# Optimization experiments

Measured on AMD Instinct MI355X. Metric: run time of the kernel, lower is better.

The kernel has to match this reference:

```python
import jax, jax.numpy as jnp
import numpy as np

N = 4096
D = 2048
NUM_CLASSES = 128
MARGIN = 0.5


def setup_inputs() -> dict:
    key = jax.random.key(0)
    k1, k2, k3 = jax.random.split(key, 3)
    modal1_inputs = jax.random.normal(k1, (N, D), dtype=jnp.float32)
    modal2_inputs = jax.random.normal(k2, (N, D), dtype=jnp.float32)
    targets = jax.random.randint(k3, (N,), 0, NUM_CLASSES, dtype=jnp.int32)
    return {"modal1_inputs": modal1_inputs, "modal2_inputs": modal2_inputs, "targets": targets}


def _segment_mean(x, seg_ids, num_segments):
    sums = jax.ops.segment_sum(x, seg_ids, num_segments=num_segments)
    cnts = jax.ops.segment_sum(jnp.ones((x.shape[0],), x.dtype), seg_ids, num_segments=num_segments)
    return sums / jnp.maximum(cnts, 1.0)[:, None]


def _pairwise_dist(a, b):
    # sqrt of clamped squared Euclidean distance, matching compute_dist
    sq = (jnp.sum(a * a, axis=1)[:, None] + jnp.sum(b * b, axis=1)[None, :]
          - 2.0 * jnp.einsum('nd,md->nm', a, b))
    return jnp.sqrt(jnp.maximum(sq, 1e-12))


def _contrastive(d2, d1, label, margin):
    # mean(label * d2^2 + (1-label) * relu(margin - d1)^2)
    return jnp.mean(label * d2 * d2
                    + (1.0 - label) * jnp.square(jnp.maximum(margin - d1, 0.0)))


def reference(modal1_inputs, modal2_inputs, targets):
    # per-label means (segment mean), gathered back per-sample as in the loop
    meanR = _segment_mean(modal1_inputs, targets, NUM_CLASSES)  # [C, D]
    meanT = _segment_mean(modal2_inputs, targets, NUM_CLASSES)  # [C, D]
    centersR = meanR[targets]                                   # [N, D]
    centersT = meanT[targets]                                   # [N, D]
    centers = 0.5 * (centersR + centersT)                       # [N, D]

    label = (targets[:, None] == targets[None, :]).astype(jnp.float32)  # [N, N]

    dist1 = _pairwise_dist(centersR, centers)  # already sqrt'ed, per original
    dist2 = _pairwise_dist(centersT, centers)
    dd1 = jnp.sqrt(dist1 + 1e-10)              # sqrt of sqrt, per original
    dd2 = jnp.sqrt(dist2 + 1e-10)

    loss1 = _contrastive(dist1, dd1, label, MARGIN)
    loss2 = _contrastive(dist2, dd2, label, MARGIN)
    return loss1 + loss2
```

## Files before the change

kernel.cpp:

```cpp
#include <hip/hip_runtime.h>

#define N_SAMPLES 4096
#define DIM 2048
#define NUM_CLASSES 128
#define MARGIN 0.5f


__global__ __launch_bounds__(256) void mean_kernel(
        const float* __restrict__ x1,
        const float* __restrict__ x2,
        const int* __restrict__ targets,
        int* __restrict__ cnt,
        float* __restrict__ meanR,
        float* __restrict__ meanT,
        float* __restrict__ d_out, int out_size) {
    __shared__ int s_rows[N_SAMPLES];
    __shared__ int s_n;
    const int tid = threadIdx.x;
    const int c = blockIdx.y;
    const float* __restrict__ x = (blockIdx.z == 0) ? x1 : x2;
    float* __restrict__ mean    = (blockIdx.z == 0) ? meanR : meanT;

    if (tid == 0) s_n = 0;
    if (blockIdx.x == 0 && blockIdx.y == 0 && blockIdx.z == 0) {
        for (int i = tid; i < out_size; i += 256) d_out[i] = 0.0f;
    }
    __syncthreads();

    const int4* __restrict__ t4 = (const int4*)targets;
    for (int i = tid; i < N_SAMPLES / 4; i += 256) {
        const int4 v = t4[i];
        const int base = i * 4;
        if (v.x == c) s_rows[atomicAdd(&s_n, 1)] = base;
        if (v.y == c) s_rows[atomicAdd(&s_n, 1)] = base + 1;
        if (v.z == c) s_rows[atomicAdd(&s_n, 1)] = base + 2;
        if (v.w == c) s_rows[atomicAdd(&s_n, 1)] = base + 3;
    }
    __syncthreads();
    const int n = s_n;

    const int col = blockIdx.x * 256 + tid;
    const float4* __restrict__ xs = (const float4*)x;
    float ax = 0.0f, ay = 0.0f, az = 0.0f, aw = 0.0f;
    int k = 0;
    for (; k + 4 <= n; k += 4) {
        const int r0 = s_rows[k + 0];
        const int r1 = s_rows[k + 1];
        const int r2 = s_rows[k + 2];
        const int r3 = s_rows[k + 3];
        const float4 v0 = xs[(size_t)r0 * (DIM / 4) + col];
        const float4 v1 = xs[(size_t)r1 * (DIM / 4) + col];
        const float4 v2 = xs[(size_t)r2 * (DIM / 4) + col];
        const float4 v3 = xs[(size_t)r3 * (DIM / 4) + col];
        ax += (v0.x + v1.x) + (v2.x + v3.x);
        ay += (v0.y + v1.y) + (v2.y + v3.y);
        az += (v0.z + v1.z) + (v2.z + v3.z);
        aw += (v0.w + v1.w) + (v2.w + v3.w);
    }
    for (; k < n; ++k) {
        const int r = s_rows[k];
        const float4 v = xs[(size_t)r * (DIM / 4) + col];
        ax += v.x; ay += v.y; az += v.z; aw += v.w;
    }
    const float inv = 1.0f / (float)((n > 0) ? n : 1);
    float4 m; m.x = ax * inv; m.y = ay * inv; m.z = az * inv; m.w = aw * inv;
    ((float4*)mean)[(size_t)c * (DIM / 4) + col] = m;

    if (blockIdx.x == 0 && blockIdx.z == 0 && tid == 0) cnt[c] = n;
}

__device__ __forceinline__ void accum_sq(float& acc, const float4& a, const float4& c) {
    float d;
    d = a.x - c.x; acc = fmaf(d, d, acc);
    d = a.y - c.y; acc = fmaf(d, d, acc);
    d = a.z - c.z; acc = fmaf(d, d, acc);
    d = a.w - c.w; acc = fmaf(d, d, acc);
}

__device__ __forceinline__ float wave_sum64(float v) {
#pragma unroll
    for (int m = 32; m >= 1; m >>= 1) v += __shfl_xor(v, m, 64);
    return v;
}

__global__ __launch_bounds__(256) void loss_kernel(
        const float* __restrict__ meanR,
        const float* __restrict__ meanT,
        const int* __restrict__ cnt,
        float* __restrict__ d_out) {
    const int gtid = blockIdx.x * blockDim.x + threadIdx.x;
    const int wid  = gtid >> 6;
    const int lane = threadIdx.x & 63;
    const int a0 = (wid >> 5) * 4;
    const int b0 = (wid & 31) * 4;

    float acc1[4][4], acc2[4][4];
#pragma unroll
    for (int i = 0; i < 4; ++i)
#pragma unroll
        for (int j = 0; j < 4; ++j) { acc1[i][j] = 0.0f; acc2[i][j] = 0.0f; }

    const int ITERS = DIM / 4 / 64;
#pragma unroll 2
    for (int it = 0; it < ITERS; ++it) {
        const int d = lane + it * 64;
        float4 ra[4], ta[4];
#pragma unroll
        for (int i = 0; i < 4; ++i) {
            ra[i] = ((const float4*)(meanR + (size_t)(a0 + i) * DIM))[d];
            ta[i] = ((const float4*)(meanT + (size_t)(a0 + i) * DIM))[d];
        }
#pragma unroll
        for (int j = 0; j < 4; ++j) {
            const int b = b0 + j;
            const float4 rb = ((const float4*)(meanR + (size_t)b * DIM))[d];
            const float4 tb = ((const float4*)(meanT + (size_t)b * DIM))[d];
            float4 cb;
            cb.x = 0.5f * (rb.x + tb.x);
            cb.y = 0.5f * (rb.y + tb.y);
            cb.z = 0.5f * (rb.z + tb.z);
            cb.w = 0.5f * (rb.w + tb.w);
#pragma unroll
            for (int i = 0; i < 4; ++i) {
                accum_sq(acc1[i][j], ra[i], cb);
                accum_sq(acc2[i][j], ta[i], cb);
            }
        }
    }

#pragma unroll
    for (int i = 0; i < 4; ++i)
#pragma unroll
        for (int j = 0; j < 4; ++j) {
            acc1[i][j] = wave_sum64(acc1[i][j]);
            acc2[i][j] = wave_sum64(acc2[i][j]);
        }

    __shared__ float s_part[4];
    if (lane == 0) {
        const float invN2 = 1.0f / ((float)N_SAMPLES * (float)N_SAMPLES);
        float total = 0.0f;
#pragma unroll
        for (int i = 0; i < 4; ++i) {
            const int a = a0 + i;
            const float ca = (float)cnt[a];
#pragma unroll
            for (int j = 0; j < 4; ++j) {
                const int b = b0 + j;
                const float w = ca * (float)cnt[b] * invN2;
                const float sq1 = fmaxf(acc1[i][j], 1e-12f);
                const float sq2 = fmaxf(acc2[i][j], 1e-12f);
                float t1, t2;
                if (a == b) {
                    t1 = sq1;
                    t2 = sq2;
                } else {
                    const float dd1 = sqrtf(sqrtf(sq1) + 1e-10f);
                    const float dd2 = sqrtf(sqrtf(sq2) + 1e-10f);
                    const float r1 = fmaxf(MARGIN - dd1, 0.0f);
                    const float r2 = fmaxf(MARGIN - dd2, 0.0f);
                    t1 = r1 * r1;
                    t2 = r2 * r2;
                }
                total += w * (t1 + t2);
            }
        }
        s_part[threadIdx.x >> 6] = total;
    }
    __syncthreads();
    if (threadIdx.x == 0)
        atomicAdd(d_out, (s_part[0] + s_part[1]) + (s_part[2] + s_part[3]));
}

extern "C" void kernel_launch(void* const* d_in, const int* in_sizes, int n_in,
                              void* d_out, int out_size, void* d_ws, size_t ws_size,
                              hipStream_t stream) {
    const float* modal1 = (const float*)d_in[0];
    const float* modal2 = (const float*)d_in[1];
    const int* targets  = (const int*)d_in[2];
    float* out = (float*)d_out;

    char* ws = (char*)d_ws;
    int*   cnt   = (int*)(ws + 0);
    float* meanR = (float*)(ws + 1024);
    float* meanT = (float*)(ws + 1024 + (size_t)NUM_CLASSES * DIM * 4);

    dim3 gridB(2, NUM_CLASSES, 2);
    mean_kernel<<<gridB, 256, 0, stream>>>(modal1, modal2, targets, cnt,
                                           meanR, meanT, out, out_size);

    const int waves = (NUM_CLASSES / 4) * (NUM_CLASSES / 4);
    loss_kernel<<<waves / 4, 256, 0, stream>>>(meanR, meanT, cnt, out);
}
```

Baseline: 119.7 us.

## Software-pipeline mean gather loads and split loss tiles across block waves

The mean kernel's gather loop now processes eight rows per step and issues the next group's loads before summing the current group, so more memory requests are in flight per thread. The loss kernel gives each 4x4 class tile its own block, splits the feature dimension across four waves, and combines the partial sums through shared memory. This launches four times as many blocks, each doing a quarter of the reduction work, which improves occupancy and latency hiding. The cost is more registers in the mean kernel plus an extra shared-memory reduction and barrier per block.

New measurement: 115.4 us. 3.6% less time.

```diff
diff --git a/kernel.cpp b/kernel.cpp
--- a/kernel.cpp
+++ b/kernel.cpp
@@ -42,26 +42,56 @@
     const int col = blockIdx.x * 256 + tid;
     const float4* __restrict__ xs = (const float4*)x;
     float ax = 0.0f, ay = 0.0f, az = 0.0f, aw = 0.0f;
+
     int k = 0;
-    for (; k + 4 <= n; k += 4) {
-        const int r0 = s_rows[k + 0];
-        const int r1 = s_rows[k + 1];
-        const int r2 = s_rows[k + 2];
-        const int r3 = s_rows[k + 3];
-        const float4 v0 = xs[(size_t)r0 * (DIM / 4) + col];
-        const float4 v1 = xs[(size_t)r1 * (DIM / 4) + col];
-        const float4 v2 = xs[(size_t)r2 * (DIM / 4) + col];
-        const float4 v3 = xs[(size_t)r3 * (DIM / 4) + col];
-        ax += (v0.x + v1.x) + (v2.x + v3.x);
-        ay += (v0.y + v1.y) + (v2.y + v3.y);
-        az += (v0.z + v1.z) + (v2.z + v3.z);
-        aw += (v0.w + v1.w) + (v2.w + v3.w);
+    const int body = n & ~7;
+    if (body >= 8) {
+        int r0 = s_rows[0], r1 = s_rows[1], r2 = s_rows[2], r3 = s_rows[3];
+        int r4 = s_rows[4], r5 = s_rows[5], r6 = s_rows[6], r7 = s_rows[7];
+        float4 v0 = xs[(size_t)r0 * (DIM / 4) + col];
+        float4 v1 = xs[(size_t)r1 * (DIM / 4) + col];
+        float4 v2 = xs[(size_t)r2 * (DIM / 4) + col];
+        float4 v3 = xs[(size_t)r3 * (DIM / 4) + col];
+        float4 v4 = xs[(size_t)r4 * (DIM / 4) + col];
+        float4 v5 = xs[(size_t)r5 * (DIM / 4) + col];
+        float4 v6 = xs[(size_t)r6 * (DIM / 4) + col];
+        float4 v7 = xs[(size_t)r7 * (DIM / 4) + col];
+
+#pragma unroll 1
+        for (k = 8; k + 8 <= body; k += 8) {
+            const int q0 = s_rows[k + 0], q1 = s_rows[k + 1];
+            const int q2 = s_rows[k + 2], q3 = s_rows[k + 3];
+            const int q4 = s_rows[k + 4], q5 = s_rows[k + 5];
+            const int q6 = s_rows[k + 6], q7 = s_rows[k + 7];
+            const float4 w0 = xs[(size_t)q0 * (DIM / 4) + col];
+            const float4 w1 = xs[(size_t)q1 * (DIM / 4) + col];
+            const float4 w2 = xs[(size_t)q2 * (DIM / 4) + col];
+            const float4 w3 = xs[(size_t)q3 * (DIM / 4) + col];
+            const float4 w4 = xs[(size_t)q4 * (DIM / 4) + col];
+            const float4 w5 = xs[(size_t)q5 * (DIM / 4) + col];
+            const float4 w6 = xs[(size_t)q6 * (DIM / 4) + col];
+            const float4 w7 = xs[(size_t)q7 * (DIM / 4) + col];
+
+            ax += ((v0.x + v1.x) + (v2.x + v3.x)) + ((v4.x + v5.x) + (v6.x + v7.x));
+            ay += ((v0.y + v1.y) + (v2.y + v3.y)) + ((v4.y + v5.y) + (v6.y + v7.y));
+            az += ((v0.z + v1.z) + (v2.z + v3.z)) + ((v4.z + v5.z) + (v6.z + v7.z));
+            aw += ((v0.w + v1.w) + (v2.w + v3.w)) + ((v4.w + v5.w) + (v6.w + v7.w));
+
+            v0 = w0; v1 = w1; v2 = w2; v3 = w3;
+            v4 = w4; v5 = w5; v6 = w6; v7 = w7;
+        }
+        ax += ((v0.x + v1.x) + (v2.x + v3.x)) + ((v4.x + v5.x) + (v6.x + v7.x));
+        ay += ((v0.y + v1.y) + (v2.y + v3.y)) + ((v4.y + v5.y) + (v6.y + v7.y));
+        az += ((v0.z + v1.z) + (v2.z + v3.z)) + ((v4.z + v5.z) + (v6.z + v7.z));
+        aw += ((v0.w + v1.w) + (v2.w + v3.w)) + ((v4.w + v5.w) + (v6.w + v7.w));
+        k = body;
     }
     for (; k < n; ++k) {
         const int r = s_rows[k];
         const float4 v = xs[(size_t)r * (DIM / 4) + col];
         ax += v.x; ay += v.y; az += v.z; aw += v.w;
     }
+
     const float inv = 1.0f / (float)((n > 0) ? n : 1);
     float4 m; m.x = ax * inv; m.y = ay * inv; m.z = az * inv; m.w = aw * inv;
     ((float4*)mean)[(size_t)c * (DIM / 4) + col] = m;
@@ -88,11 +118,11 @@
         const float* __restrict__ meanT,
         const int* __restrict__ cnt,
         float* __restrict__ d_out) {
-    const int gtid = blockIdx.x * blockDim.x + threadIdx.x;
-    const int wid  = gtid >> 6;
+    const int tile = blockIdx.x;
+    const int a0 = (tile >> 5) * 4;
+    const int b0 = (tile & 31) * 4;
+    const int wave = threadIdx.x >> 6;
     const int lane = threadIdx.x & 63;
-    const int a0 = (wid >> 5) * 4;
-    const int b0 = (wid & 31) * 4;
 
     float acc1[4][4], acc2[4][4];
 #pragma unroll
@@ -100,10 +130,9 @@
 #pragma unroll
         for (int j = 0; j < 4; ++j) { acc1[i][j] = 0.0f; acc2[i][j] = 0.0f; }
 
-    const int ITERS = DIM / 4 / 64;
-#pragma unroll 2
-    for (int it = 0; it < ITERS; ++it) {
-        const int d = lane + it * 64;
+#pragma unroll
+    for (int it = 0; it < 2; ++it) {
+        const int d = wave * 128 + it * 64 + lane;
         float4 ra[4], ta[4];
 #pragma unroll
         for (int i = 0; i < 4; ++i) {
@@ -136,40 +165,47 @@
             acc2[i][j] = wave_sum64(acc2[i][j]);
         }
 
-    __shared__ float s_part[4];
+    __shared__ float s1[4][16], s2[4][16];
     if (lane == 0) {
-        const float invN2 = 1.0f / ((float)N_SAMPLES * (float)N_SAMPLES);
+#pragma unroll
+        for (int i = 0; i < 4; ++i)
+#pragma unroll
+            for (int j = 0; j < 4; ++j) {
+                s1[wave][i * 4 + j] = acc1[i][j];
+                s2[wave][i * 4 + j] = acc2[i][j];
+            }
+    }
+    __syncthreads();
+
+    if (threadIdx.x < 64) {
         float total = 0.0f;
-#pragma unroll
-        for (int i = 0; i < 4; ++i) {
-            const int a = a0 + i;
-            const float ca = (float)cnt[a];
-#pragma unroll
-            for (int j = 0; j < 4; ++j) {
-                const int b = b0 + j;
-                const float w = ca * (float)cnt[b] * invN2;
-                const float sq1 = fmaxf(acc1[i][j], 1e-12f);
-                const float sq2 = fmaxf(acc2[i][j], 1e-12f);
-                float t1, t2;
-                if (a == b) {
-                    t1 = sq1;
-                    t2 = sq2;
-                } else {
-                    const float dd1 = sqrtf(sqrtf(sq1) + 1e-10f);
-                    const float dd2 = sqrtf(sqrtf(sq2) + 1e-10f);
-                    const float r1 = fmaxf(MARGIN - dd1, 0.0f);
-                    const float r2 = fmaxf(MARGIN - dd2, 0.0f);
-                    t1 = r1 * r1;
-                    t2 = r2 * r2;
-                }
-                total += w * (t1 + t2);
+        if (threadIdx.x < 16) {
+            const int idx = threadIdx.x;
+            const int i = idx >> 2, j = idx & 3;
+            const int a = a0 + i, b = b0 + j;
+            const float sqa1 = (s1[0][idx] + s1[1][idx]) + (s1[2][idx] + s1[3][idx]);
+            const float sqa2 = (s2[0][idx] + s2[1][idx]) + (s2[2][idx] + s2[3][idx]);
+            const float invN2 = 1.0f / ((float)N_SAMPLES * (float)N_SAMPLES);
+            const float w = (float)cnt[a] * (float)cnt[b] * invN2;
+            const float sq1 = fmaxf(sqa1, 1e-12f);
+            const float sq2 = fmaxf(sqa2, 1e-12f);
+            float t1, t2;
+            if (a == b) {
+                t1 = sq1;
+                t2 = sq2;
+            } else {
+                const float dd1 = sqrtf(sqrtf(sq1) + 1e-10f);
+                const float dd2 = sqrtf(sqrtf(sq2) + 1e-10f);
+                const float r1 = fmaxf(MARGIN - dd1, 0.0f);
+                const float r2 = fmaxf(MARGIN - dd2, 0.0f);
+                t1 = r1 * r1;
+                t2 = r2 * r2;
             }
-        }
-        s_part[threadIdx.x >> 6] = total;
-    }
-    __syncthreads();
-    if (threadIdx.x == 0)
-        atomicAdd(d_out, (s_part[0] + s_part[1]) + (s_part[2] + s_part[3]));
+            total = w * (t1 + t2);
+        }
+        total = wave_sum64(total);
+        if (threadIdx.x == 0) atomicAdd(d_out, total);
+    }
 }
 
 extern "C" void kernel_launch(void* const* d_in, const int* in_sizes, int n_in,
@@ -189,6 +225,6 @@
     mean_kernel<<<gridB, 256, 0, stream>>>(modal1, modal2, targets, cnt,
                                            meanR, meanT, out, out_size);
 
-    const int waves = (NUM_CLASSES / 4) * (NUM_CLASSES / 4);
-    loss_kernel<<<waves / 4, 256, 0, stream>>>(meanR, meanT, cnt, out);
-}
+    loss_kernel<<<NUM_CLASSES / 4 * NUM_CLASSES / 4, 256, 0, stream>>>(
+        meanR, meanT, cnt, out);
+}
```
